# Optimization experiments

Hardware: AMD Instinct MI355X
Metric: run time of the kernel (lower is better)

Reference implementation:

```python
import jax, jax.numpy as jnp
import numpy as np

B, L, D, H = 4, 2048, 1024, 64  # batch, seq, d_model, head_size

def setup_inputs() -> dict:
    key = jax.random.key(0)
    k1, k2 = jax.random.split(key)
    x = jax.random.normal(k1, (B, L, D), dtype=jnp.float32)
    # nn.Linear(d_model, head_size, bias=False) weight: [head_size, d_model]
    Wq = jax.random.normal(k2, (H, D), dtype=jnp.float32) * (1.0 / np.sqrt(D))
    return {"x": x, "Wq": Wq}

def reference(x, Wq):
    # Faithful to source bug: q, k, v ALL use the query projection.
    q = jnp.einsum('bld,hd->blh', x, Wq)
    k = q
    v = q
    d_k = x.shape[-1]  # source uses d_model, not head_size
    scores = jnp.einsum('blh,bmh->blm', q, k) / jnp.sqrt(jnp.float32(d_k))
    Lq = x.shape[1]
    causal = jnp.tril(jnp.ones((Lq, Lq), dtype=bool))
    scores = jnp.where(causal, scores, -jnp.inf)
    attn = jax.nn.softmax(scores, axis=-1)
    # dropout in eval mode -> identity
    return jnp.einsum('blm,bmh->blh', attn, v)
```

## Files before the change

### kernel.cpp

```cpp
#include <hip/hip_runtime.h>
#include <cmath>

#define Bb 4
#define Ll 2048
#define Dd 1024
#define Hh 64

typedef float f32x4 __attribute__((ext_vector_type(4)));
typedef short s16x8 __attribute__((ext_vector_type(8)));

__device__ __forceinline__ unsigned short f2bf(float f) {
    union { float f; unsigned int u; } v; v.f = f;
    unsigned int u = v.u;
    return (unsigned short)((u + 0x7FFFu + ((u >> 16) & 1u)) >> 16);
}
__device__ __forceinline__ unsigned int pack2(float a, float b) {
    return (unsigned int)f2bf(a) | ((unsigned int)f2bf(b) << 16);
}

__global__ __launch_bounds__(256) void wq_cvt(const float* __restrict__ Wq,
                                              unsigned short* __restrict__ wqb) {
    const int i = (blockIdx.x * 256 + threadIdx.x) * 8;
    float4 a = *(const float4*)(Wq + i);
    float4 b = *(const float4*)(Wq + i + 4);
    uint4 p; p.x = pack2(a.x, a.y); p.y = pack2(a.z, a.w);
    p.z = pack2(b.x, b.y); p.w = pack2(b.z, b.w);
    *(uint4*)(wqb + i) = p;
}

__global__ __launch_bounds__(256, 2) void proj_mfma(const float* __restrict__ x,
                                                    const unsigned short* __restrict__ wqb,
                                                    unsigned short* __restrict__ q,
                                                    unsigned short* __restrict__ qT) {
    __shared__ uint4 xs4[32 * 16];
    __shared__ uint4 ws4[32 * 64];
    const int t = threadIdx.x;
    const int lane = t & 63;
    const int w = t >> 6;
    const int m15 = lane & 15;
    const int q_ = lane >> 4;
    const int row0 = blockIdx.x * 16;

    f32x4 acc = {0.f, 0.f, 0.f, 0.f};

    for (int k0 = 0; k0 < Dd; k0 += 256) {
        __syncthreads();
#pragma unroll
        for (int j = 0; j < 2; ++j) {
            int idx = t + j * 256;
            int r = idx >> 5, kc = idx & 31;
            const float* src = x + (size_t)(row0 + r) * Dd + k0 + kc * 8;
            float4 a = *(const float4*)src;
            float4 b = *(const float4*)(src + 4);
            uint4 p; p.x = pack2(a.x, a.y); p.y = pack2(a.z, a.w);
            p.z = pack2(b.x, b.y); p.w = pack2(b.z, b.w);
            xs4[kc * 16 + (r ^ (kc & 15))] = p;
        }
#pragma unroll
        for (int j = 0; j < 8; ++j) {
            int idx = t + j * 256;
            int h = idx >> 5, kc = idx & 31;
            ws4[kc * 64 + (h ^ kc)] = *(const uint4*)(wqb + (size_t)h * Dd + k0 + kc * 8);
        }
        __syncthreads();
#pragma unroll
        for (int ks = 0; ks < 8; ++ks) {
            int kc = ks * 4 + q_;
            s16x8 A = *(const s16x8*)&xs4[kc * 16 + (m15 ^ (kc & 15))];
            s16x8 B = *(const s16x8*)&ws4[kc * 64 + ((w * 16 + m15) ^ kc)];
            acc = __builtin_amdgcn_mfma_f32_16x16x32_bf16(A, B, acc, 0, 0, 0);
        }
    }
    const int h = w * 16 + m15;
    const int b = row0 >> 11;
    const int mloc = (row0 & 2047) + q_ * 4;
    unsigned short u0 = f2bf(acc[0]), u1 = f2bf(acc[1]), u2 = f2bf(acc[2]), u3 = f2bf(acc[3]);
    q[(size_t)(row0 + q_ * 4 + 0) * Hh + h] = u0;
    q[(size_t)(row0 + q_ * 4 + 1) * Hh + h] = u1;
    q[(size_t)(row0 + q_ * 4 + 2) * Hh + h] = u2;
    q[(size_t)(row0 + q_ * 4 + 3) * Hh + h] = u3;
    ushort4 pk; pk.x = u0; pk.y = u1; pk.z = u2; pk.w = u3;
    *(ushort4*)&qT[((size_t)(b * Hh + h)) * Ll + mloc] = pk;
}

__global__ __launch_bounds__(256, 3) void flash_mfma(const unsigned short* __restrict__ qg,
                                                     const unsigned short* __restrict__ qTg,
                                                     float* __restrict__ PO,
                                                     float* __restrict__ ML) {
    const int qt = blockIdx.x;
    const int s  = blockIdx.y;
    const int b  = blockIdx.z;
    if (s > (qt >> 2)) return;
    __shared__ uint4 Qs4[512], Ks4[512], Vt4[512];
    __shared__ __align__(16) unsigned short Pb[4 * 16 * 72];
    const int t = threadIdx.x, lane = t & 63, w = t >> 6;
    const int m15 = lane & 15, q_ = lane >> 4;
    const unsigned short* qb  = qg  + (size_t)b * Ll * Hh;
    const unsigned short* qTb = qTg + (size_t)b * Hh * Ll;

#pragma unroll
    for (int j = 0; j < 2; ++j) {
        int idx = t + j * 256;
        int r = idx >> 3, hc = idx & 7;
        Qs4[hc * 64 + (r ^ hc)] = *(const uint4*)(qb + (size_t)(qt * 64 + r) * Hh + hc * 8);
    }
    f32x4 Oacc[4];
#pragma unroll
    for (int i = 0; i < 4; ++i) Oacc[i] = (f32x4){0.f, 0.f, 0.f, 0.f};
    float mr = -INFINITY, lr = 0.f;
    const int n_it = min(4, qt - 4 * s + 1);
    const int c_base = s * 256;
    const int row = qt * 64 + w * 16 + m15;
    unsigned short* Pr = Pb + (w * 16 + m15) * 72;

    for (int it = 0; it < n_it; ++it) {
        const int c0 = c_base + it * 64;
        __syncthreads();
#pragma unroll
        for (int j = 0; j < 2; ++j) {
            int idx = t + j * 256;
            int c = idx >> 3, hc = idx & 7;
            Ks4[hc * 64 + (c ^ hc)] = *(const uint4*)(qb + (size_t)(c0 + c) * Hh + hc * 8);
        }
#pragma unroll
        for (int j = 0; j < 2; ++j) {
            int idx = t + j * 256;
            int h = idx >> 3, cc = idx & 7;
            Vt4[cc * 64 + (h ^ cc)] = *(const uint4*)(qTb + (size_t)h * Ll + c0 + cc * 8);
        }
        __syncthreads();
        f32x4 sc[4];
#pragma unroll
        for (int ct = 0; ct < 4; ++ct) sc[ct] = (f32x4){0.f, 0.f, 0.f, 0.f};
#pragma unroll
        for (int ks = 0; ks < 2; ++ks) {
            int hc = ks * 4 + q_;
            s16x8 Bq = *(const s16x8*)&Qs4[hc * 64 + ((w * 16 + m15) ^ hc)];
#pragma unroll
            for (int ct = 0; ct < 4; ++ct) {
                s16x8 Ak = *(const s16x8*)&Ks4[hc * 64 + ((ct * 16 + m15) ^ hc)];
                sc[ct] = __builtin_amdgcn_mfma_f32_16x16x32_bf16(Ak, Bq, sc[ct], 0, 0, 0);
            }
        }
        const bool diag = (4 * s + it) == qt;
        float v[16];
#pragma unroll
        for (int ct = 0; ct < 4; ++ct)
#pragma unroll
            for (int r = 0; r < 4; ++r) {
                float sv = sc[ct][r] * 0.03125f;
                if (diag && (c0 + ct * 16 + q_ * 4 + r > row)) sv = -INFINITY;
                v[ct * 4 + r] = sv;
            }
        float vmax = v[0];
#pragma unroll
        for (int i = 1; i < 16; ++i) vmax = fmaxf(vmax, v[i]);
        vmax = fmaxf(vmax, __shfl_xor(vmax, 16, 64));
        vmax = fmaxf(vmax, __shfl_xor(vmax, 32, 64));
        float mnew = fmaxf(mr, vmax);
        float alpha = __expf(mr - mnew);
        float p[16];
        float psum = 0.f;
#pragma unroll
        for (int i = 0; i < 16; ++i) { p[i] = __expf(v[i] - mnew); psum += p[i]; }
        psum += __shfl_xor(psum, 16, 64);
        psum += __shfl_xor(psum, 32, 64);
        lr = lr * alpha + psum;
        mr = mnew;
#pragma unroll
        for (int ht = 0; ht < 4; ++ht) Oacc[ht] *= alpha;
#pragma unroll
        for (int ct = 0; ct < 4; ++ct) {
            uint2 pr; pr.x = pack2(p[ct * 4 + 0], p[ct * 4 + 1]);
            pr.y = pack2(p[ct * 4 + 2], p[ct * 4 + 3]);
            *(uint2*)(Pr + ct * 16 + q_ * 4) = pr;
        }
#pragma unroll
        for (int kc = 0; kc < 2; ++kc) {
            int cc = kc * 4 + q_;
            s16x8 Bp = *(const s16x8*)(Pr + kc * 32 + q_ * 8);
#pragma unroll
            for (int ht = 0; ht < 4; ++ht) {
                s16x8 Av = *(const s16x8*)&Vt4[cc * 64 + ((ht * 16 + m15) ^ cc)];
                Oacc[ht] = __builtin_amdgcn_mfma_f32_16x16x32_bf16(Av, Bp, Oacc[ht], 0, 0, 0);
            }
        }
    }
    const size_t base = ((size_t)((b * 32 + qt) * 8 + s)) * 4096;
#pragma unroll
    for (int ht = 0; ht < 4; ++ht)
        *(f32x4*)&PO[base + (size_t)(w * 16 + m15) * 64 + ht * 16 + q_ * 4] = Oacc[ht];
    if (q_ == 0) {
        float* mlp = ML + ((size_t)((b * 32 + qt) * 8 + s)) * 128;
        mlp[(w * 16 + m15) * 2 + 0] = mr;
        mlp[(w * 16 + m15) * 2 + 1] = lr;
    }
}

__global__ __launch_bounds__(256) void combine_k(const float* __restrict__ PO,
                                                 const float* __restrict__ ML,
                                                 float* __restrict__ out) {
    const int bq = blockIdx.x;
    const int b = bq >> 5, qt = bq & 31;
    const int ns = (qt >> 2) + 1;
    const int t = threadIdx.x;
    const int r = blockIdx.y * 32 + (t >> 3);
    const int c8 = (t & 7) * 8;
    const float* mlp = ML + (size_t)bq * 8 * 128;
    const float* pob = PO + (size_t)bq * 8 * 4096;
    float M = -INFINITY;
    for (int si = 0; si < ns; ++si) M = fmaxf(M, mlp[si * 128 + r * 2]);
    float L = 0.f;
    f32x4 a0 = {0.f, 0.f, 0.f, 0.f}, a1 = a0;
    for (int si = 0; si < ns; ++si) {
        float ms = mlp[si * 128 + r * 2], ls = mlp[si * 128 + r * 2 + 1];
        float wgt = __expf(ms - M);
        L += ls * wgt;
        const f32x4* sp = (const f32x4*)(pob + (size_t)si * 4096 + r * 64 + c8);
        a0 += wgt * sp[0];
        a1 += wgt * sp[1];
    }
    float inv = 1.0f / L;
    f32x4* op = (f32x4*)(out + (size_t)(b * Ll + qt * 64 + r) * 64 + c8);
    op[0] = a0 * inv;
    op[1] = a1 * inv;
}

extern "C" void kernel_launch(void* const* d_in, const int* in_sizes, int n_in,
                              void* d_out, int out_size, void* d_ws, size_t ws_size,
                              hipStream_t stream) {
    const float* x  = (const float*)d_in[0];
    const float* Wq = (const float*)d_in[1];
    float* out = (float*)d_out;
    char* ws = (char*)d_ws;
    unsigned short* q   = (unsigned short*)ws;
    unsigned short* qT  = (unsigned short*)(ws + (1 << 20));
    float* PO = (float*)(ws + (2 << 20));
    float* ML = (float*)(ws + (18 << 20));
    unsigned short* wqb = (unsigned short*)(ws + (19 << 20));

    wq_cvt<<<32, 256, 0, stream>>>(Wq, wqb);
    proj_mfma<<<512, 256, 0, stream>>>(x, wqb, q, qT);
    flash_mfma<<<dim3(32, 8, Bb), 256, 0, stream>>>(q, qT, PO, ML);
    combine_k<<<dim3(128, 2), 256, 0, stream>>>(PO, ML, out);
}
```

Measured before the change: 102.3 us.

## Pre-swizzle Q/K/V layouts, double-buffer with direct-to-LDS loads, fold softmax scale

The projection kernel now writes q and qT already in the swizzled tile layout that the attention kernel uses. Whole tiles can then be copied with global_load_lds straight into LDS, and the converted Wq is pre-swizzled the same way. Both the projection and flash kernels double-buffer their LDS tiles, so the next chunk's loads overlap the current MFMA work. Other changes: the scale and log2(e) factor are folded into q so the softmax can use exp2 with no per-score multiply, bf16 conversion uses the hardware packed-convert instruction, and s_setprio is raised around the MFMA blocks. The main risk is correctness of the asynchronous LDS loads: the flash loop relies on a single barrier, and the compiler must insert the wait for those loads.

```diff
diff --git a/kernel.cpp b/kernel.cpp
--- a/kernel.cpp
+++ b/kernel.cpp
@@ -6,81 +6,124 @@
 #define Dd 1024
 #define Hh 64
 
+#define QSCL 0.21233050f
+
 typedef float f32x4 __attribute__((ext_vector_type(4)));
 typedef short s16x8 __attribute__((ext_vector_type(8)));
 
-__device__ __forceinline__ unsigned short f2bf(float f) {
-    union { float f; unsigned int u; } v; v.f = f;
-    unsigned int u = v.u;
-    return (unsigned short)((u + 0x7FFFu + ((u >> 16) & 1u)) >> 16);
-}
-__device__ __forceinline__ unsigned int pack2(float a, float b) {
-    return (unsigned int)f2bf(a) | ((unsigned int)f2bf(b) << 16);
+__device__ __forceinline__ unsigned int cvtpk(float a, float b) {
+    unsigned int r;
+    asm("v_cvt_pk_bf16_f32 %0, %1, %2" : "=v"(r) : "v"(a), "v"(b));
+    return r;
+}
+
+__device__ __forceinline__ void gload16(const void* g, void* l) {
+    __builtin_amdgcn_global_load_lds((__attribute__((address_space(1))) const void*)g,
+                                     (__attribute__((address_space(3))) void*)l, 16, 0, 0);
 }
 
 __global__ __launch_bounds__(256) void wq_cvt(const float* __restrict__ Wq,
                                               unsigned short* __restrict__ wqb) {
-    const int i = (blockIdx.x * 256 + threadIdx.x) * 8;
-    float4 a = *(const float4*)(Wq + i);
-    float4 b = *(const float4*)(Wq + i + 4);
-    uint4 p; p.x = pack2(a.x, a.y); p.y = pack2(a.z, a.w);
-    p.z = pack2(b.x, b.y); p.w = pack2(b.z, b.w);
-    *(uint4*)(wqb + i) = p;
+    const int idx = blockIdx.x * 256 + threadIdx.x;
+    const int c   = idx >> 11;
+    const int kc  = (idx >> 6) & 31;
+    const int hsw = idx & 63;
+    const int h   = hsw ^ kc;
+    const float* src = Wq + (size_t)h * Dd + c * 256 + kc * 8;
+    float4 a = *(const float4*)src;
+    float4 b = *(const float4*)(src + 4);
+    uint4 p; p.x = cvtpk(a.x, a.y); p.y = cvtpk(a.z, a.w);
+    p.z = cvtpk(b.x, b.y); p.w = cvtpk(b.z, b.w);
+    *(uint4*)(wqb + (size_t)idx * 8) = p;
 }
 
 __global__ __launch_bounds__(256, 2) void proj_mfma(const float* __restrict__ x,
                                                     const unsigned short* __restrict__ wqb,
                                                     unsigned short* __restrict__ q,
                                                     unsigned short* __restrict__ qT) {
-    __shared__ uint4 xs4[32 * 16];
-    __shared__ uint4 ws4[32 * 64];
+    __shared__ uint4 xs4[2][32 * 16];
+    __shared__ uint4 ws4[2][32 * 64];
     const int t = threadIdx.x;
-    const int lane = t & 63;
-    const int w = t >> 6;
-    const int m15 = lane & 15;
-    const int q_ = lane >> 4;
+    const int lane = t & 63, w = t >> 6;
+    const int m15 = lane & 15, q_ = lane >> 4;
     const int row0 = blockIdx.x * 16;
+    const int kc = t & 31, rr = t >> 5;
+    const float* xsrc0 = x + (size_t)(row0 + rr) * Dd + kc * 8;
+    const float* xsrc1 = x + (size_t)(row0 + rr + 8) * Dd + kc * 8;
+
+    float4 xa0 = *(const float4*)xsrc0, xb0 = *(const float4*)(xsrc0 + 4);
+    float4 xa1 = *(const float4*)xsrc1, xb1 = *(const float4*)(xsrc1 + 4);
+#pragma unroll
+    for (int j = 0; j < 8; ++j) {
+        int off = t + j * 256;
+        gload16(wqb + (size_t)off * 8, (char*)ws4[0] + off * 16);
+    }
+    {
+        uint4 p0; p0.x = cvtpk(xa0.x, xa0.y); p0.y = cvtpk(xa0.z, xa0.w);
+        p0.z = cvtpk(xb0.x, xb0.y); p0.w = cvtpk(xb0.z, xb0.w);
+        xs4[0][kc * 16 + (rr ^ (kc & 15))] = p0;
+        uint4 p1; p1.x = cvtpk(xa1.x, xa1.y); p1.y = cvtpk(xa1.z, xa1.w);
+        p1.z = cvtpk(xb1.x, xb1.y); p1.w = cvtpk(xb1.z, xb1.w);
+        xs4[0][kc * 16 + ((rr + 8) ^ (kc & 15))] = p1;
+    }
+    xa0 = *(const float4*)(xsrc0 + 256); xb0 = *(const float4*)(xsrc0 + 260);
+    xa1 = *(const float4*)(xsrc1 + 256); xb1 = *(const float4*)(xsrc1 + 260);
 
     f32x4 acc = {0.f, 0.f, 0.f, 0.f};
-
-    for (int k0 = 0; k0 < Dd; k0 += 256) {
+    for (int c = 0; c < 4; ++c) {
+        const int p = c & 1;
         __syncthreads();
-#pragma unroll
-        for (int j = 0; j < 2; ++j) {
-            int idx = t + j * 256;
-            int r = idx >> 5, kc = idx & 31;
-            const float* src = x + (size_t)(row0 + r) * Dd + k0 + kc * 8;
-            float4 a = *(const float4*)src;
-            float4 b = *(const float4*)(src + 4);
-            uint4 p; p.x = pack2(a.x, a.y); p.y = pack2(a.z, a.w);
-            p.z = pack2(b.x, b.y); p.w = pack2(b.z, b.w);
-            xs4[kc * 16 + (r ^ (kc & 15))] = p;
-        }
-#pragma unroll
-        for (int j = 0; j < 8; ++j) {
-            int idx = t + j * 256;
-            int h = idx >> 5, kc = idx & 31;
-            ws4[kc * 64 + (h ^ kc)] = *(const uint4*)(wqb + (size_t)h * Dd + k0 + kc * 8);
-        }
-        __syncthreads();
+        if (c + 1 < 4) {
+#pragma unroll
+            for (int j = 0; j < 8; ++j) {
+                int off = t + j * 256;
+                gload16(wqb + (size_t)(c + 1) * 16384 + (size_t)off * 8,
+                        (char*)ws4[p ^ 1] + off * 16);
+            }
+            uint4 p0; p0.x = cvtpk(xa0.x, xa0.y); p0.y = cvtpk(xa0.z, xa0.w);
+            p0.z = cvtpk(xb0.x, xb0.y); p0.w = cvtpk(xb0.z, xb0.w);
+            xs4[p ^ 1][kc * 16 + (rr ^ (kc & 15))] = p0;
+            uint4 p1; p1.x = cvtpk(xa1.x, xa1.y); p1.y = cvtpk(xa1.z, xa1.w);
+            p1.z = cvtpk(xb1.x, xb1.y); p1.w = cvtpk(xb1.z, xb1.w);
+            xs4[p ^ 1][kc * 16 + ((rr + 8) ^ (kc & 15))] = p1;
+            if (c + 2 < 4) {
+                xa0 = *(const float4*)(xsrc0 + (c + 2) * 256);
+                xb0 = *(const float4*)(xsrc0 + (c + 2) * 256 + 4);
+                xa1 = *(const float4*)(xsrc1 + (c + 2) * 256);
+                xb1 = *(const float4*)(xsrc1 + (c + 2) * 256 + 4);
+            }
+        }
 #pragma unroll
         for (int ks = 0; ks < 8; ++ks) {
-            int kc = ks * 4 + q_;
-            s16x8 A = *(const s16x8*)&xs4[kc * 16 + (m15 ^ (kc & 15))];
-            s16x8 B = *(const s16x8*)&ws4[kc * 64 + ((w * 16 + m15) ^ kc)];
+            int kk = ks * 4 + q_;
+            s16x8 A = *(const s16x8*)&xs4[p][kk * 16 + (m15 ^ (kk & 15))];
+            s16x8 B = *(const s16x8*)&ws4[p][kk * 64 + ((w * 16 + m15) ^ kk)];
             acc = __builtin_amdgcn_mfma_f32_16x16x32_bf16(A, B, acc, 0, 0, 0);
         }
     }
     const int h = w * 16 + m15;
+    const int hc = h >> 3, he = h & 7;
+    const size_t T = (size_t)(row0 >> 6);
+    const int rbase = (row0 & 63) + q_ * 4;
+    unsigned int a01 = cvtpk(acc[0] * QSCL, acc[1] * QSCL);
+    unsigned int a23 = cvtpk(acc[2] * QSCL, acc[3] * QSCL);
+    unsigned short u[4] = { (unsigned short)(a01 & 0xFFFF), (unsigned short)(a01 >> 16),
+                            (unsigned short)(a23 & 0xFFFF), (unsigned short)(a23 >> 16) };
+#pragma unroll
+    for (int i = 0; i < 4; ++i) {
+        int rsw = (rbase + i) ^ hc;
+        q[((T * 8 + hc) * 64 + rsw) * 8 + he] = u[i];
+    }
+    unsigned int t01 = cvtpk(acc[0], acc[1]);
+    unsigned int t23 = cvtpk(acc[2], acc[3]);
     const int b = row0 >> 11;
-    const int mloc = (row0 & 2047) + q_ * 4;
-    unsigned short u0 = f2bf(acc[0]), u1 = f2bf(acc[1]), u2 = f2bf(acc[2]), u3 = f2bf(acc[3]);
-    q[(size_t)(row0 + q_ * 4 + 0) * Hh + h] = u0;
-    q[(size_t)(row0 + q_ * 4 + 1) * Hh + h] = u1;
-    q[(size_t)(row0 + q_ * 4 + 2) * Hh + h] = u2;
-    q[(size_t)(row0 + q_ * 4 + 3) * Hh + h] = u3;
-    ushort4 pk; pk.x = u0; pk.y = u1; pk.z = u2; pk.w = u3;
-    *(ushort4*)&qT[((size_t)(b * Hh + h)) * Ll + mloc] = pk;
+    const int m0 = (row0 & 2047) + q_ * 4;
+    const int vt = m0 >> 6, cc = (m0 >> 3) & 7, me = m0 & 7;
+    const int hsw = h ^ cc;
+    ushort4 pk4;
+    pk4.x = (unsigned short)(t01 & 0xFFFF); pk4.y = (unsigned short)(t01 >> 16);
+    pk4.z = (unsigned short)(t23 & 0xFFFF); pk4.w = (unsigned short)(t23 >> 16);
+    *(ushort4*)&qT[(((size_t)(b * 32 + vt) * 8 + cc) * 64 + hsw) * 8 + me] = pk4;
 }
 
 __global__ __launch_bounds__(256, 3) void flash_mfma(const unsigned short* __restrict__ qg,
@@ -91,78 +134,91 @@
     const int s  = blockIdx.y;
     const int b  = blockIdx.z;
     if (s > (qt >> 2)) return;
-    __shared__ uint4 Qs4[512], Ks4[512], Vt4[512];
+    __shared__ uint4 Qs4[512];
+    __shared__ uint4 Ks4[2][512];
+    __shared__ uint4 Vt4[2][512];
     __shared__ __align__(16) unsigned short Pb[4 * 16 * 72];
     const int t = threadIdx.x, lane = t & 63, w = t >> 6;
     const int m15 = lane & 15, q_ = lane >> 4;
-    const unsigned short* qb  = qg  + (size_t)b * Ll * Hh;
-    const unsigned short* qTb = qTg + (size_t)b * Hh * Ll;
+    const int n_it = min(4, qt - 4 * s + 1);
+    const int tb = b * 32;
+    const unsigned short* qsrc = qg + (size_t)(tb + qt) * 4096;
 
 #pragma unroll
     for (int j = 0; j < 2; ++j) {
-        int idx = t + j * 256;
-        int r = idx >> 3, hc = idx & 7;
-        Qs4[hc * 64 + (r ^ hc)] = *(const uint4*)(qb + (size_t)(qt * 64 + r) * Hh + hc * 8);
+        int off = t + j * 256;
+        gload16(qsrc + (size_t)off * 8, (char*)Qs4 + off * 16);
+        gload16(qg  + (size_t)(tb + s * 4) * 4096 + (size_t)off * 8, (char*)Ks4[0] + off * 16);
+        gload16(qTg + (size_t)(tb + s * 4) * 4096 + (size_t)off * 8, (char*)Vt4[0] + off * 16);
     }
     f32x4 Oacc[4];
 #pragma unroll
     for (int i = 0; i < 4; ++i) Oacc[i] = (f32x4){0.f, 0.f, 0.f, 0.f};
     float mr = -INFINITY, lr = 0.f;
-    const int n_it = min(4, qt - 4 * s + 1);
-    const int c_base = s * 256;
-    const int row = qt * 64 + w * 16 + m15;
     unsigned short* Pr = Pb + (w * 16 + m15) * 72;
 
     for (int it = 0; it < n_it; ++it) {
-        const int c0 = c_base + it * 64;
+        const int pp = it & 1;
         __syncthreads();
-#pragma unroll
-        for (int j = 0; j < 2; ++j) {
-            int idx = t + j * 256;
-            int c = idx >> 3, hc = idx & 7;
-            Ks4[hc * 64 + (c ^ hc)] = *(const uint4*)(qb + (size_t)(c0 + c) * Hh + hc * 8);
-        }
-#pragma unroll
-        for (int j = 0; j < 2; ++j) {
-            int idx = t + j * 256;
-            int h = idx >> 3, cc = idx & 7;
-            Vt4[cc * 64 + (h ^ cc)] = *(const uint4*)(qTb + (size_t)h * Ll + c0 + cc * 8);
-        }
-        __syncthreads();
+        if (it + 1 < n_it) {
+            const unsigned short* k2 = qg  + (size_t)(tb + s * 4 + it + 1) * 4096;
+            const unsigned short* v2 = qTg + (size_t)(tb + s * 4 + it + 1) * 4096;
+#pragma unroll
+            for (int j = 0; j < 2; ++j) {
+                int off = t + j * 256;
+                gload16(k2 + (size_t)off * 8, (char*)Ks4[pp ^ 1] + off * 16);
+                gload16(v2 + (size_t)off * 8, (char*)Vt4[pp ^ 1] + off * 16);
+            }
+        }
         f32x4 sc[4];
 #pragma unroll
         for (int ct = 0; ct < 4; ++ct) sc[ct] = (f32x4){0.f, 0.f, 0.f, 0.f};
+        __builtin_amdgcn_s_setprio(1);
 #pragma unroll
         for (int ks = 0; ks < 2; ++ks) {
-            int hc = ks * 4 + q_;
+            const int hc = ks * 4 + q_;
             s16x8 Bq = *(const s16x8*)&Qs4[hc * 64 + ((w * 16 + m15) ^ hc)];
 #pragma unroll
             for (int ct = 0; ct < 4; ++ct) {
-                s16x8 Ak = *(const s16x8*)&Ks4[hc * 64 + ((ct * 16 + m15) ^ hc)];
+                s16x8 Ak = *(const s16x8*)&Ks4[pp][hc * 64 + ((ct * 16 + m15) ^ hc)];
                 sc[ct] = __builtin_amdgcn_mfma_f32_16x16x32_bf16(Ak, Bq, sc[ct], 0, 0, 0);
             }
         }
+        __builtin_amdgcn_s_setprio(0);
+
         const bool diag = (4 * s + it) == qt;
         float v[16];
-#pragma unroll
-        for (int ct = 0; ct < 4; ++ct)
-#pragma unroll
-            for (int r = 0; r < 4; ++r) {
-                float sv = sc[ct][r] * 0.03125f;
-                if (diag && (c0 + ct * 16 + q_ * 4 + r > row)) sv = -INFINITY;
-                v[ct * 4 + r] = sv;
-            }
-        float vmax = v[0];
-#pragma unroll
-        for (int i = 1; i < 16; ++i) vmax = fmaxf(vmax, v[i]);
+        if (diag) {
+            const int rel = w * 16 + m15 - q_ * 4;
+#pragma unroll
+            for (int ct = 0; ct < 4; ++ct)
+#pragma unroll
+                for (int r = 0; r < 4; ++r)
+                    v[ct * 4 + r] = (ct * 16 + r > rel) ? -INFINITY : sc[ct][r];
+        } else {
+#pragma unroll
+            for (int ct = 0; ct < 4; ++ct)
+#pragma unroll
+                for (int r = 0; r < 4; ++r)
+                    v[ct * 4 + r] = sc[ct][r];
+        }
+        float x01 = fmaxf(v[0], v[1]),  x23 = fmaxf(v[2], v[3]);
+        float x45 = fmaxf(v[4], v[5]),  x67 = fmaxf(v[6], v[7]);
+        float x89 = fmaxf(v[8], v[9]),  xab = fmaxf(v[10], v[11]);
+        float xcd = fmaxf(v[12], v[13]), xef = fmaxf(v[14], v[15]);
+        float vmax = fmaxf(fmaxf(fmaxf(x01, x23), fmaxf(x45, x67)),
+                           fmaxf(fmaxf(x89, xab), fmaxf(xcd, xef)));
         vmax = fmaxf(vmax, __shfl_xor(vmax, 16, 64));
         vmax = fmaxf(vmax, __shfl_xor(vmax, 32, 64));
-        float mnew = fmaxf(mr, vmax);
-        float alpha = __expf(mr - mnew);
-        float p[16];
-        float psum = 0.f;
-#pragma unroll
-        for (int i = 0; i < 16; ++i) { p[i] = __expf(v[i] - mnew); psum += p[i]; }
+        const float mnew = fmaxf(mr, vmax);
+        const float alpha = exp2f(mr - mnew);
+#pragma unroll
+        for (int i = 0; i < 16; ++i) v[i] = exp2f(v[i] - mnew);
+        float s01 = (v[0] + v[1]) + (v[2] + v[3]);
+        float s23 = (v[4] + v[5]) + (v[6] + v[7]);
+        float s45 = (v[8] + v[9]) + (v[10] + v[11]);
+        float s67 = (v[12] + v[13]) + (v[14] + v[15]);
+        float psum = (s01 + s23) + (s45 + s67);
         psum += __shfl_xor(psum, 16, 64);
         psum += __shfl_xor(psum, 32, 64);
         lr = lr * alpha + psum;
@@ -171,20 +227,22 @@
         for (int ht = 0; ht < 4; ++ht) Oacc[ht] *= alpha;
 #pragma unroll
         for (int ct = 0; ct < 4; ++ct) {
-            uint2 pr; pr.x = pack2(p[ct * 4 + 0], p[ct * 4 + 1]);
-            pr.y = pack2(p[ct * 4 + 2], p[ct * 4 + 3]);
+            uint2 pr; pr.x = cvtpk(v[ct * 4 + 0], v[ct * 4 + 1]);
+            pr.y = cvtpk(v[ct * 4 + 2], v[ct * 4 + 3]);
             *(uint2*)(Pr + ct * 16 + q_ * 4) = pr;
         }
-#pragma unroll
-        for (int kc = 0; kc < 2; ++kc) {
-            int cc = kc * 4 + q_;
-            s16x8 Bp = *(const s16x8*)(Pr + kc * 32 + q_ * 8);
+        __builtin_amdgcn_s_setprio(1);
+#pragma unroll
+        for (int kc2 = 0; kc2 < 2; ++kc2) {
+            const int cc = kc2 * 4 + q_;
+            s16x8 Bp = *(const s16x8*)(Pr + kc2 * 32 + q_ * 8);
 #pragma unroll
             for (int ht = 0; ht < 4; ++ht) {
-                s16x8 Av = *(const s16x8*)&Vt4[cc * 64 + ((ht * 16 + m15) ^ cc)];
+                s16x8 Av = *(const s16x8*)&Vt4[pp][cc * 64 + ((ht * 16 + m15) ^ cc)];
                 Oacc[ht] = __builtin_amdgcn_mfma_f32_16x16x32_bf16(Av, Bp, Oacc[ht], 0, 0, 0);
             }
         }
+        __builtin_amdgcn_s_setprio(0);
     }
     const size_t base = ((size_t)((b * 32 + qt) * 8 + s)) * 4096;
 #pragma unroll
@@ -214,7 +272,7 @@
     f32x4 a0 = {0.f, 0.f, 0.f, 0.f}, a1 = a0;
     for (int si = 0; si < ns; ++si) {
         float ms = mlp[si * 128 + r * 2], ls = mlp[si * 128 + r * 2 + 1];
-        float wgt = __expf(ms - M);
+        float wgt = exp2f(ms - M);
         L += ls * wgt;
         const f32x4* sp = (const f32x4*)(pob + (size_t)si * 4096 + r * 64 + c8);
         a0 += wgt * sp[0];
```

Measured after the change: 103.0 us. No clear change (+0.7%).
